# Kernel optimization log

Measured on AMD Instinct MI355X. Metric: run time of the kernel, lower is better.

## Reference

```python
import jax, jax.numpy as jnp
import numpy as np

NUM_NODES = 100000
NUM_EDGES = 1200000
IN_CH = 64
HID_CH = 64
NUM_REL = 8
DEG = NUM_EDGES // NUM_NODES  # uniform degree 12


def setup_inputs() -> dict:
    key = jax.random.key(0)
    k1, k2, k3, k4 = jax.random.split(key, 4)
    x = jax.random.normal(k1, (NUM_NODES, IN_CH), dtype=jnp.float32)
    linear = jax.random.normal(k2, (NUM_REL, IN_CH, HID_CH), dtype=jnp.float32) * (1.0 / np.sqrt(IN_CH))
    ptr = jnp.arange(NUM_NODES + 1, dtype=jnp.int64) * DEG  # CSR row pointers, uniform degree
    idx = jax.random.randint(k3, (NUM_EDGES,), 0, NUM_NODES, dtype=jnp.int64)
    edge_types = jax.random.randint(k4, (NUM_EDGES,), 0, NUM_REL, dtype=jnp.int64)
    return {"x": x, "linear": linear, "ptr": ptr, "idx": idx,
            "edge_types": edge_types, "num_node": NUM_NODES}


def reference(x, linear, ptr, idx, edge_types, num_node):
    # Gather source-node features per edge: [E, in]
    gathered = x[idx]
    # Per-edge-type linear transform (loop over small fixed num_rel, like RGCNOP)
    out_e = jnp.zeros((gathered.shape[0], linear.shape[-1]), dtype=gathered.dtype)
    for r in range(linear.shape[0]):
        mask = (edge_types == r).astype(gathered.dtype)[:, None]
        out_e = out_e + mask * (gathered @ linear[r])
    # CSR scatter-sum aggregation over destination segments defined by ptr
    num_edges = idx.shape[0]
    seg_ids = jnp.searchsorted(ptr, jnp.arange(num_edges, dtype=ptr.dtype), side='right') - 1
    agg = jax.ops.segment_sum(out_e, seg_ids, num_segments=num_node)
    # Degree normalization
    deg = (ptr[1:] - ptr[:-1]).astype(agg.dtype)
    return agg / deg[:, None]
```

## Files before the change

kernel.cpp:

```cpp
#include <hip/hip_runtime.h>
#include <hip/hip_bf16.h>


#define THREADS 512
#define NPB 32
#define KDIM 512
#define LDA 520
#define MAXE 512
#define WFRAG (4 * 16 * 64 * 8)

typedef __attribute__((ext_vector_type(8))) short bf16x8;
typedef __attribute__((ext_vector_type(4))) float f32x4;

extern __shared__ __align__(16) char smem[];

__device__ __forceinline__ unsigned short f2bf(float f) {
  __hip_bfloat16 h = __float2bfloat16(f);
  return *reinterpret_cast<unsigned short*>(&h);
}

__global__ __launch_bounds__(256) void pack_w(const void* __restrict__ wv,
                                              unsigned short* __restrict__ wsB) {
  const int lane = threadIdx.x & 63;
  const unsigned word = ((const unsigned*)wv)[lane];
  const int exf = (int)((word >> 7) & 0xFFu);
  const bool w_bf16 = __popcll(__ballot(exf >= 96 && exf < 160)) >= 48;
  for (int i = blockIdx.x * 256 + threadIdx.x; i < WFRAG; i += gridDim.x * 256) {
    const int j  = i & 7;
    const int l  = (i >> 3) & 63;
    const int kt = (i >> 9) & 15;
    const int nt = i >> 13;
    const int k  = kt * 32 + (l >> 4) * 8 + j;
    const int n  = nt * 16 + (l & 15);
    float v;
    if (w_bf16) v = __bfloat162float(((const __hip_bfloat16*)wv)[k * 64 + n]);
    else        v = ((const float*)wv)[k * 64 + n];
    wsB[i] = f2bf(v);
  }
}

#define ACC_SW(accrow, r, vv)                                        \
  switch (r) {                                                       \
    case 0: accrow[0] += (vv); break; case 1: accrow[1] += (vv); break; \
    case 2: accrow[2] += (vv); break; case 3: accrow[3] += (vv); break; \
    case 4: accrow[4] += (vv); break; case 5: accrow[5] += (vv); break; \
    case 6: accrow[6] += (vv); break; default: accrow[7] += (vv); break; }

__global__ __launch_bounds__(THREADS, 8)
void rgcn_fused(const void* __restrict__ xv,
                const void* __restrict__ wv,
                const int* __restrict__ p32,
                const int* __restrict__ i32,
                const int* __restrict__ t32,
                const unsigned short* __restrict__ wsB,
                float* __restrict__ out,
                int num_nodes) {
  __hip_bfloat16* aggS = (__hip_bfloat16*)smem;
  __hip_bfloat16* wtS  = aggS + NPB * LDA;
  char* tail = smem + (size_t)NPB * LDA * 2 + (wsB ? 0 : (size_t)64 * LDA * 2);
  float*    invS  = (float*)tail;
  int*      ptrS  = (int*)(tail + 256);
  unsigned* eMeta = (unsigned*)(tail + 256 + 144);

  const int tid   = threadIdx.x;
  const int lane  = tid & 63;
  const int wvid  = tid >> 6;
  const int node0 = blockIdx.x * NPB;

  const unsigned xword = ((const unsigned*)xv)[lane];
  const int exf = (int)((xword >> 7) & 0xFFu);
  const bool x_bf16 = __popcll(__ballot(exf >= 96 && exf < 160)) >= 48;
  const bool idx64 = (p32[1] == 0);

  auto ldptr = [&](int n) -> int { return idx64 ? p32[2 * n] : p32[n]; };

  const int ntop   = min(node0 + NPB, num_nodes);
  const int e_lo   = ldptr(node0);
  const int ecount = ldptr(ntop) - e_lo;
  const bool staged = (ecount > 0 && ecount <= MAXE);

  for (int i = tid; i <= NPB; i += THREADS)
    ptrS[i] = ldptr(min(node0 + i, num_nodes));

  if (staged) {
    for (int e = tid; e < ecount; e += THREADS) {
      const int ge = e_lo + e;
      const unsigned s = (unsigned)(idx64 ? i32[2 * ge] : i32[ge]);
      const unsigned r = (unsigned)(idx64 ? t32[2 * ge] : t32[ge]);
      eMeta[e] = s | (r << 24);
    }
  }

  if (!wsB) {
    if (x_bf16) {
      const __hip_bfloat16* wb = (const __hip_bfloat16*)wv;
      for (int i = tid; i < KDIM * 64; i += THREADS)
        wtS[(i & 63) * LDA + (i >> 6)] = wb[i];
    } else {
      const float* wf = (const float*)wv;
      for (int i = tid; i < KDIM * 64; i += THREADS)
        wtS[(i & 63) * LDA + (i >> 6)] = __float2bfloat16(wf[i]);
    }
  }

  __syncthreads();

  for (int i = tid; i < NPB; i += THREADS) {
    const int d = ptrS[i + 1] - ptrS[i];
    invS[i] = (d > 0 && node0 + i < num_nodes) ? 1.0f / (float)d : 0.0f;
  }

  auto gather = [&](auto lc) {
    for (int t = 0; t < 4; ++t) {
      const int nl  = wvid * 4 + t;
      const int pe0 = __builtin_amdgcn_readfirstlane(ptrS[nl]);
      const int pe1 = __builtin_amdgcn_readfirstlane(ptrS[nl + 1]);
      const int e0  = pe0 - e_lo;
      const int dg  = pe1 - pe0;
      const bool inb = (node0 + nl < num_nodes);
      if (staged && inb && dg == 12) {
        int m[12];
#pragma unroll
        for (int j = 0; j < 12; ++j)
          m[j] = __builtin_amdgcn_readfirstlane((int)eMeta[e0 + j]);
        float v[12];
#pragma unroll
        for (int j = 0; j < 12; ++j)
          v[j] = lc((int)((unsigned)m[j] & 0x00FFFFFFu));
        float acc[8] = {0.f, 0.f, 0.f, 0.f, 0.f, 0.f, 0.f, 0.f};
#pragma unroll
        for (int j = 0; j < 12; ++j) {
          const int r = (int)((unsigned)m[j] >> 24);
          ACC_SW(acc, r, v[j])
        }
#pragma unroll
        for (int r = 0; r < 8; ++r)
          aggS[nl * LDA + r * 64 + lane] = __float2bfloat16(acc[r]);
      } else {
        float a[8] = {0.f, 0.f, 0.f, 0.f, 0.f, 0.f, 0.f, 0.f};
        if (inb) {
          const int ee0 = pe0 - e_lo, ee1 = pe1 - e_lo;
          for (int e = ee0; e < ee1; ++e) {
            unsigned mm;
            if (staged) mm = eMeta[e];
            else {
              const int ge = e_lo + e;
              mm = (unsigned)(idx64 ? i32[2 * ge] : i32[ge]) |
                   ((unsigned)(idx64 ? t32[2 * ge] : t32[ge]) << 24);
            }
            const float vv = lc((int)(mm & 0x00FFFFFFu));
            const int r = __builtin_amdgcn_readfirstlane((int)(mm >> 24));
            ACC_SW(a, r, vv)
          }
        }
#pragma unroll
        for (int r = 0; r < 8; ++r)
          aggS[nl * LDA + r * 64 + lane] = __float2bfloat16(a[r]);
      }
    }
  };

  if (x_bf16) {
    auto lc = [&](int s) -> float {
      const unsigned short u = ((const unsigned short*)xv)[((size_t)s << 6) + lane];
      return __uint_as_float((unsigned)u << 16);
    };
    gather(lc);
  } else {
    auto lc = [&](int s) -> float {
      return ((const float*)xv)[((size_t)s << 6) + lane];
    };
    gather(lc);
  }

  __syncthreads();

  const int mt = wvid >> 2;
  const int nt = wvid & 3;
  const int mi = lane & 15;
  const int q4 = lane >> 4;
  const __hip_bfloat16* ap = aggS + (mt * 16 + mi) * LDA + q4 * 8;
  f32x4 c0 = {0.f, 0.f, 0.f, 0.f};
  if (wsB) {
    const bf16x8* B = (const bf16x8*)wsB;
#pragma unroll
    for (int kt = 0; kt < KDIM / 32; ++kt) {
      const bf16x8 a = *(const bf16x8*)(ap + kt * 32);
      const bf16x8 b = B[(nt * 16 + kt) * 64 + lane];
      c0 = __builtin_amdgcn_mfma_f32_16x16x32_bf16(a, b, c0, 0, 0, 0);
    }
  } else {
    const __hip_bfloat16* bp = wtS + (nt * 16 + mi) * LDA + q4 * 8;
#pragma unroll
    for (int kt = 0; kt < KDIM / 32; ++kt) {
      const bf16x8 a = *(const bf16x8*)(ap + kt * 32);
      const bf16x8 b = *(const bf16x8*)(bp + kt * 32);
      c0 = __builtin_amdgcn_mfma_f32_16x16x32_bf16(a, b, c0, 0, 0, 0);
    }
  }

#pragma unroll
  for (int i = 0; i < 4; ++i) {
    const int row  = q4 * 4 + i;
    const int nl   = mt * 16 + row;
    const int node = node0 + nl;
    if (node < num_nodes) {
      out[(size_t)node * 64 + nt * 16 + mi] = c0[i] * invS[nl];
    }
  }
}

extern "C" void kernel_launch(void* const* d_in, const int* in_sizes, int n_in,
                              void* d_out, int out_size, void* d_ws, size_t ws_size,
                              hipStream_t stream) {
  const void* x   = d_in[0];
  const void* w   = d_in[1];
  const int*  ptr = (const int*)d_in[2];
  const int*  idx = (const int*)d_in[3];
  const int*  et  = (const int*)d_in[4];
  float*      out = (float*)d_out;

  const int num_nodes = in_sizes[0] / 64;

  const bool useWs = (d_ws != nullptr) &&
                     (ws_size >= (size_t)WFRAG * sizeof(unsigned short));
  unsigned short* wsB = useWs ? (unsigned short*)d_ws : nullptr;
  if (useWs) pack_w<<<32, 256, 0, stream>>>(w, wsB);

  const size_t lds_bytes = (size_t)NPB * LDA * 2 +
                           (useWs ? 0 : (size_t)64 * LDA * 2) +
                           256 + 144 + (size_t)MAXE * 4;

  hipFuncSetAttribute((const void*)rgcn_fused,
                      hipFuncAttributeMaxDynamicSharedMemorySize,
                      (int)lds_bytes);

  const int nblocks = (num_nodes + NPB - 1) / NPB;
  rgcn_fused<<<nblocks, THREADS, lds_bytes, stream>>>(x, w, ptr, idx, et, wsB,
                                                      out, num_nodes);
}
```

Measured before the change: 145.3 us.

## Gather four nodes per wavefront with 16-byte row loads and masked accumulation

Restructures the gather so each wavefront processes its four nodes at once, with 16 lanes per node each loading a 16-byte float4 chunk of a source row. This replaces four sequential passes of scalar per-lane loads. Per-relation accumulation uses mask multiplies instead of a switch, writes go out as packed ushort4 bf16, and launch bounds are relaxed from 8 to 6 waves. The change aims to raise memory-level parallelism and cut instruction count in the gather, at the cost of more registers (acc[8] as float4) and 8x redundant FMAs per edge.

```diff
diff --git a/kernel.cpp b/kernel.cpp
--- a/kernel.cpp
+++ b/kernel.cpp
@@ -46,7 +46,7 @@
     case 4: accrow[4] += (vv); break; case 5: accrow[5] += (vv); break; \
     case 6: accrow[6] += (vv); break; default: accrow[7] += (vv); break; }
 
-__global__ __launch_bounds__(THREADS, 8)
+__global__ __launch_bounds__(THREADS, 6)
 void rgcn_fused(const void* __restrict__ xv,
                 const void* __restrict__ wv,
                 const int* __restrict__ p32,
@@ -110,37 +110,55 @@
     invS[i] = (d > 0 && node0 + i < num_nodes) ? 1.0f / (float)d : 0.0f;
   }
 
-  auto gather = [&](auto lc) {
-    for (int t = 0; t < 4; ++t) {
-      const int nl  = wvid * 4 + t;
-      const int pe0 = __builtin_amdgcn_readfirstlane(ptrS[nl]);
-      const int pe1 = __builtin_amdgcn_readfirstlane(ptrS[nl + 1]);
-      const int e0  = pe0 - e_lo;
-      const int dg  = pe1 - pe0;
-      const bool inb = (node0 + nl < num_nodes);
-      if (staged && inb && dg == 12) {
-        int m[12];
-#pragma unroll
-        for (int j = 0; j < 12; ++j)
-          m[j] = __builtin_amdgcn_readfirstlane((int)eMeta[e0 + j]);
-        float v[12];
-#pragma unroll
-        for (int j = 0; j < 12; ++j)
-          v[j] = lc((int)((unsigned)m[j] & 0x00FFFFFFu));
-        float acc[8] = {0.f, 0.f, 0.f, 0.f, 0.f, 0.f, 0.f, 0.f};
-#pragma unroll
-        for (int j = 0; j < 12; ++j) {
-          const int r = (int)((unsigned)m[j] >> 24);
-          ACC_SW(acc, r, v[j])
+  const int c16 = lane & 15;
+  const int qd  = lane >> 4;
+
+  auto gather = [&](auto xp, auto loadrow) {
+    const int nlb = wvid * 4;
+    const int eq0 = ptrS[nlb + qd] - e_lo;
+    const int dq  = ptrS[nlb + qd + 1] - e_lo - eq0;
+    const bool okfast = staged && (node0 + nlb + 3 < num_nodes) &&
+                        (__ballot(dq == 12) == ~0ull);
+    if (okfast) {
+      f32x4 acc[8];
+#pragma unroll
+      for (int r = 0; r < 8; ++r) acc[r] = (f32x4){0.f, 0.f, 0.f, 0.f};
+#pragma unroll
+      for (int h = 0; h < 2; ++h) {
+        unsigned mB[6];
+#pragma unroll
+        for (int j = 0; j < 6; ++j) mB[j] = eMeta[eq0 + h * 6 + j];
+        f32x4 v[6];
+#pragma unroll
+        for (int j = 0; j < 6; ++j)
+          v[j] = loadrow((int)(mB[j] & 0x00FFFFFFu), c16);
+#pragma unroll
+        for (int j = 0; j < 6; ++j) {
+          const unsigned rj = mB[j] >> 24;
+#pragma unroll
+          for (int r = 0; r < 8; ++r) {
+            const float mk = (rj == (unsigned)r) ? 1.0f : 0.0f;
+            const f32x4 m4 = {mk, mk, mk, mk};
+            acc[r] += m4 * v[j];
+          }
         }
-#pragma unroll
-        for (int r = 0; r < 8; ++r)
-          aggS[nl * LDA + r * 64 + lane] = __float2bfloat16(acc[r]);
-      } else {
+      }
+      unsigned short* dst = (unsigned short*)(aggS + (nlb + qd) * LDA) + 4 * c16;
+#pragma unroll
+      for (int r = 0; r < 8; ++r) {
+        ushort4 b;
+        b.x = f2bf(acc[r][0]); b.y = f2bf(acc[r][1]);
+        b.z = f2bf(acc[r][2]); b.w = f2bf(acc[r][3]);
+        *(ushort4*)(dst + r * 64) = b;
+      }
+    } else {
+#pragma unroll
+      for (int t = 0; t < 4; ++t) {
+        const int nl = nlb + t;
         float a[8] = {0.f, 0.f, 0.f, 0.f, 0.f, 0.f, 0.f, 0.f};
-        if (inb) {
-          const int ee0 = pe0 - e_lo, ee1 = pe1 - e_lo;
-          for (int e = ee0; e < ee1; ++e) {
+        if (node0 + nl < num_nodes) {
+          const int e0 = ptrS[nl] - e_lo, e1 = ptrS[nl + 1] - e_lo;
+          for (int e = e0; e < e1; ++e) {
             unsigned mm;
             if (staged) mm = eMeta[e];
             else {
@@ -148,7 +166,7 @@
               mm = (unsigned)(idx64 ? i32[2 * ge] : i32[ge]) |
                    ((unsigned)(idx64 ? t32[2 * ge] : t32[ge]) << 24);
             }
-            const float vv = lc((int)(mm & 0x00FFFFFFu));
+            const float vv = (float)xp[(size_t)(mm & 0x00FFFFFFu) * 64 + lane];
             const int r = __builtin_amdgcn_readfirstlane((int)(mm >> 24));
             ACC_SW(a, r, vv)
           }
@@ -161,16 +179,23 @@
   };
 
   if (x_bf16) {
-    auto lc = [&](int s) -> float {
-      const unsigned short u = ((const unsigned short*)xv)[((size_t)s << 6) + lane];
-      return __uint_as_float((unsigned)u << 16);
+    const __hip_bfloat16* xb = (const __hip_bfloat16*)xv;
+    auto lr = [&](int src, int c) -> f32x4 {
+      const ushort4 u = ((const ushort4*)xv)[(size_t)src * 16 + c];
+      f32x4 f;
+      f[0] = __uint_as_float((unsigned)(unsigned short)u.x << 16);
+      f[1] = __uint_as_float((unsigned)(unsigned short)u.y << 16);
+      f[2] = __uint_as_float((unsigned)(unsigned short)u.z << 16);
+      f[3] = __uint_as_float((unsigned)(unsigned short)u.w << 16);
+      return f;
     };
-    gather(lc);
+    gather(xb, lr);
   } else {
-    auto lc = [&](int s) -> float {
-      return ((const float*)xv)[((size_t)s << 6) + lane];
+    const float* xf = (const float*)xv;
+    auto lr = [&](int src, int c) -> f32x4 {
+      return ((const f32x4*)xv)[(size_t)src * 16 + c];
     };
-    gather(lc);
+    gather(xf, lr);
   }
 
   __syncthreads();
```

After: 134.3 us. 7.6% less time.
